# Kernel optimization log

Measured on AMD Instinct MI355X. Metric: run time of the kernel, lower is better.

## Reference

```python
import jax, jax.numpy as jnp
import numpy as np

S, I, CM, C, D, CZ = 128, 512, 256, 32, 32, 128
EPS = 1e-5


def setup_inputs() -> dict:
    key = jax.random.key(0)
    ks = jax.random.split(key, 7)
    x = jax.random.normal(ks[0], (1, S, I, CM), dtype=jnp.float32)
    norm_w = 1.0 + 0.1 * jax.random.normal(ks[1], (CM,), dtype=jnp.float32)
    norm_b = 0.1 * jax.random.normal(ks[2], (CM,), dtype=jnp.float32)
    Wa = jax.random.normal(ks[3], (C, CM), dtype=jnp.float32) / np.sqrt(CM)
    Wb = jax.random.normal(ks[4], (D, CM), dtype=jnp.float32) / np.sqrt(CM)
    Wo = jax.random.normal(ks[5], (CZ, C * D), dtype=jnp.float32) / np.sqrt(C * D)
    bo = 0.1 * jax.random.normal(ks[6], (CZ,), dtype=jnp.float32)
    return {"x": x, "norm_w": norm_w, "norm_b": norm_b, "Wa": Wa, "Wb": Wb, "Wo": Wo, "bo": bo}


def reference(x, norm_w, norm_b, Wa, Wb, Wo, bo):
    m = x[0]                                   # [S, I, CM] (drop leading batch dim)
    mu = jnp.mean(m, axis=-1, keepdims=True)
    var = jnp.mean((m - mu) ** 2, axis=-1, keepdims=True)
    ln = (m - mu) * jax.lax.rsqrt(var + EPS) * norm_w + norm_b
    a = jnp.einsum('sim,cm->sic', ln, Wa)      # [S, I, C]
    b = jnp.einsum('sjm,dm->sjd', ln, Wb)      # [S, J, D]
    s = a.shape[0]
    # outer product mean over S: [I, J, C, D]; flatten order is (c, d) -> c*D + d,
    # matching the reshape(chunk, C, J, D) -> permute(0,2,1,3) -> flatten in the original.
    o = jnp.einsum('sic,sjd->ijcd', a, b) * (1.0 / s)
    z = o.reshape(o.shape[0], o.shape[1], C * D) @ Wo.T + bo  # [I, J, CZ]
    return z[None]                             # [1, I, J, CZ]
```

## Files before the change

kernel.cpp:

```cpp
#include <hip/hip_runtime.h>

#define EPS 1e-5f

typedef _Float16 half8 __attribute__((ext_vector_type(8)));
typedef _Float16 half4 __attribute__((ext_vector_type(4)));
typedef float f32x4 __attribute__((ext_vector_type(4)));

#define AB_STRIDE 72
#define AB_CHUNK  (16384 * AB_STRIDE)

__device__ __forceinline__ void load16_to_lds(const void* g, void* l) {
    __builtin_amdgcn_global_load_lds((__attribute__((address_space(1))) void*)g,
                                     (__attribute__((address_space(3))) void*)l, 16, 0, 0);
}

__global__ void k_cvt(const float* __restrict__ Wo, const float* __restrict__ Wa,
                      const float* __restrict__ Wb, _Float16* __restrict__ WoH,
                      _Float16* __restrict__ WabH)
{
    int t = blockIdx.x * 256 + threadIdx.x;
    if (t < 32768) {
        int n  = t >> 8;
        int k4 = (t & 255) * 4;
        float4 v = *(const float4*)(Wo + (size_t)n * 1024 + k4);
        int c = k4 >> 5, d0 = k4 & 31;
        _Float16* dst = WoH + (size_t)n * 1024 + c;
        dst[(d0 + 0) * 32] = (_Float16)v.x;
        dst[(d0 + 1) * 32] = (_Float16)v.y;
        dst[(d0 + 2) * 32] = (_Float16)v.z;
        dst[(d0 + 3) * 32] = (_Float16)v.w;
    } else {
        int idx = (t - 32768) * 4;
        const float* src = (idx < 8192) ? (Wa + idx) : (Wb + (idx - 8192));
        float4 v = *(const float4*)src;
        half4 h;
        h[0] = (_Float16)v.x; h[1] = (_Float16)v.y; h[2] = (_Float16)v.z; h[3] = (_Float16)v.w;
        *(half4*)(WabH + idx) = h;
    }
}

__global__ __launch_bounds__(512, 4)
void k1_ln_proj(const float* __restrict__ x, const float* __restrict__ nw,
                const float* __restrict__ nb, const _Float16* __restrict__ WabH,
                _Float16* __restrict__ aT, _Float16* __restrict__ bT)
{
    __shared__ _Float16 xln[64 * 264];
    __shared__ _Float16 oT[256 * 72];

    const int tid  = threadIdx.x;
    const int lane = tid & 63;
    const int w    = tid >> 6;
    const int quad = lane >> 4;
    const int l15  = lane & 15;
    const int i0   = (blockIdx.x >> 1) * 4;
    const int sc   = blockIdx.x & 1;

    const int mt  = w & 3;
    const int ntg = w >> 2;

    for (int sub = 0; sub < 4; ++sub) {
        for (int rr = 0; rr < 8; ++rr) {
            int rl = w * 8 + rr;
            int s_ = sc * 64 + sub * 16 + (rl >> 2);
            int i_ = i0 + (rl & 3);
            const float4* xr = (const float4*)(x + ((size_t)s_ * 512 + i_) * 256);
            float4 v = xr[lane];
            float sum = v.x + v.y + v.z + v.w;
            float ss  = v.x * v.x + v.y * v.y + v.z * v.z + v.w * v.w;
            #pragma unroll
            for (int off = 32; off > 0; off >>= 1) {
                sum += __shfl_xor(sum, off);
                ss  += __shfl_xor(ss, off);
            }
            float mu  = sum * (1.f / 256.f);
            float var = ss * (1.f / 256.f) - mu * mu;
            float rs  = rsqrtf(var + EPS);
            float4 gw = ((const float4*)nw)[lane];
            float4 gb = ((const float4*)nb)[lane];
            half4 o;
            o[0] = (_Float16)((v.x - mu) * rs * gw.x + gb.x);
            o[1] = (_Float16)((v.y - mu) * rs * gw.y + gb.y);
            o[2] = (_Float16)((v.z - mu) * rs * gw.z + gb.z);
            o[3] = (_Float16)((v.w - mu) * rs * gw.w + gb.w);
            *(half4*)(xln + rl * 264 + lane * 4) = o;
        }
        __syncthreads();

        f32x4 acc2[2] = {};
        #pragma unroll
        for (int kk = 0; kk < 8; ++kk) {
            half8 af = *(const half8*)(xln + (mt * 16 + l15) * 264 + kk * 32 + quad * 8);
            #pragma unroll
            for (int t = 0; t < 2; ++t) {
                half8 bf = *(const half8*)(WabH + (ntg * 32 + t * 16 + l15) * 256 + kk * 32 + quad * 8);
                acc2[t] = __builtin_amdgcn_mfma_f32_16x16x32_f16(af, bf, acc2[t], 0, 0, 0);
            }
        }

        #pragma unroll
        for (int t = 0; t < 2; ++t) {
            int c64  = ntg * 32 + t * 16 + l15;
            int base = ((c64 >= 32) ? 128 : 0) + (c64 & 31);
            int s_l  = sub * 16 + mt * 4 + quad;
            #pragma unroll
            for (int r = 0; r < 4; ++r)
                oT[(base + r * 32) * 72 + s_l] = (_Float16)acc2[t][r];
        }
        __syncthreads();
    }

    #pragma unroll
    for (int it2 = 0; it2 < 4; ++it2) {
        int u   = it2 * 512 + tid;
        int row = u >> 3;
        int off = (u & 7) * 8;
        half8 v = *(const half8*)(oT + row * 72 + off);
        _Float16* dst = (row < 128) ? aT : bT;
        int grow = i0 * 32 + (row & 127);
        *(half8*)(dst + (size_t)sc * AB_CHUNK + (size_t)grow * 72 + off) = v;
    }
}

__global__ __launch_bounds__(512, 4)
void k2_main(const _Float16* __restrict__ aT, const _Float16* __restrict__ bT,
             const _Float16* __restrict__ WoH, const float* __restrict__ bo,
             float* __restrict__ out)
{
    __shared__ _Float16 smem[33024];
    _Float16* sA = smem;
    _Float16* sB = smem + 256 * AB_STRIDE;
    _Float16* oL = smem;

    const int tid  = threadIdx.x;
    const int lane = tid & 63;
    const int w    = tid >> 6;
    const int quad = lane >> 4;
    const int l15  = lane & 15;
    const int wy   = w >> 1, wx = w & 1;

    const int jt = blockIdx.x, it = blockIdx.y;
    const char* gA = (const char*)(aT + (size_t)it * 256 * AB_STRIDE);
    const char* gB = (const char*)(bT + (size_t)jt * 128 * AB_STRIDE);

    f32x4 acc[4][4] = {};

    for (int ck = 0; ck < 2; ++ck) {
        const char* cA = gA + (size_t)ck * (AB_CHUNK * 2);
        const char* cB = gB + (size_t)ck * (AB_CHUNK * 2);
        for (int seg = w; seg < 54; seg += 8) {
            if (seg < 36) load16_to_lds(cA + seg * 1024 + lane * 16, (char*)sA + seg * 1024 + lane * 16);
            else          load16_to_lds(cB + (seg - 36) * 1024 + lane * 16, (char*)sB + (seg - 36) * 1024 + lane * 16);
        }
        __syncthreads();

        #pragma unroll
        for (int kloc = 0; kloc < 2; ++kloc) {
            half8 af[4], bf[4];
            #pragma unroll
            for (int mt = 0; mt < 4; ++mt)
                af[mt] = *(const half8*)(sA + (wy * 64 + mt * 16 + l15) * AB_STRIDE + kloc * 32 + quad * 8);
            #pragma unroll
            for (int nt = 0; nt < 4; ++nt)
                bf[nt] = *(const half8*)(sB + (wx * 64 + nt * 16 + l15) * AB_STRIDE + kloc * 32 + quad * 8);
            #pragma unroll
            for (int mt = 0; mt < 4; ++mt)
                #pragma unroll
                for (int nt = 0; nt < 4; ++nt)
                    acc[mt][nt] = __builtin_amdgcn_mfma_f32_16x16x32_f16(af[mt], bf[nt], acc[mt][nt], 0, 0, 0);
        }
        __syncthreads();
    }

    #pragma unroll
    for (int mt = 0; mt < 4; ++mt) {
        int c0     = (mt & 1) * 16 + quad * 4;
        int chunk3 = (c0 >> 3);
        int il     = wy * 2 + (mt >> 1);
        #pragma unroll
        for (int nt = 0; nt < 4; ++nt) {
            int d    = (nt & 1) * 16 + l15;
            int jl   = wx * 2 + (nt >> 1);
            int pair = il * 4 + jl;
            int cS   = (c0 & 7) + ((chunk3 ^ ((d >> 1) & 3)) << 3);
            half4 v;
            v[0] = (_Float16)(acc[mt][nt][0] * (1.f / 128.f));
            v[1] = (_Float16)(acc[mt][nt][1] * (1.f / 128.f));
            v[2] = (_Float16)(acc[mt][nt][2] * (1.f / 128.f));
            v[3] = (_Float16)(acc[mt][nt][3] * (1.f / 128.f));
            *(half4*)(oL + pair * 1032 + d * 32 + cS) = v;
        }
    }
    __syncthreads();

    f32x4 zacc[2] = {};
    const int n0 = w * 16 + l15;
    #pragma unroll 4
    for (int kk = 0; kk < 32; ++kk) {
        int csw = (quad ^ ((kk >> 1) & 3)) * 8;
        half8 oa0 = *(const half8*)(oL + (l15) * 1032 + kk * 32 + csw);
        half8 oa1 = *(const half8*)(oL + (16 + l15) * 1032 + kk * 32 + csw);
        half8 w0  = *(const half8*)(WoH + (size_t)n0 * 1024 + kk * 32 + quad * 8);
        zacc[0] = __builtin_amdgcn_mfma_f32_16x16x32_f16(oa0, w0, zacc[0], 0, 0, 0);
        zacc[1] = __builtin_amdgcn_mfma_f32_16x16x32_f16(oa1, w0, zacc[1], 0, 0, 0);
    }

    float bias = bo[w * 16 + l15];
    #pragma unroll
    for (int mt2 = 0; mt2 < 2; ++mt2) {
        #pragma unroll
        for (int r = 0; r < 4; ++r) {
            int il = mt2 * 4 + quad;
            int jl = r;
            out[(((size_t)(it * 8 + il)) * 512 + jt * 4 + jl) * 128 + w * 16 + l15] = zacc[mt2][r] + bias;
        }
    }
}

extern "C" void kernel_launch(void* const* d_in, const int* in_sizes, int n_in,
                              void* d_out, int out_size, void* d_ws, size_t ws_size,
                              hipStream_t stream)
{
    const float* x      = (const float*)d_in[0];
    const float* norm_w = (const float*)d_in[1];
    const float* norm_b = (const float*)d_in[2];
    const float* Wa     = (const float*)d_in[3];
    const float* Wb     = (const float*)d_in[4];
    const float* Wo     = (const float*)d_in[5];
    const float* bo     = (const float*)d_in[6];
    float* out = (float*)d_out;

    _Float16* aT   = (_Float16*)d_ws;
    _Float16* bT   = aT + 2 * (size_t)AB_CHUNK;
    _Float16* WoH  = bT + 2 * (size_t)AB_CHUNK;
    _Float16* WabH = WoH + 131072;

    k_cvt<<<144, 256, 0, stream>>>(Wo, Wa, Wb, WoH, WabH);
    k1_ln_proj<<<256, 512, 0, stream>>>(x, norm_w, norm_b, WabH, aT, bT);
    k2_main<<<dim3(128, 64), 512, 0, stream>>>(aT, bT, WoH, bo, out);
}
```

Baseline: 485.0 us.

## Split LN-projection over more blocks, swizzle k2 grid, prefetch Wo into registers

The LN+projection kernel now gives each block one 16-row S slice instead of looping over four, which quadruples the block count and shrinks the transpose staging buffer. The main kernel becomes a 1D grid remapped into 16x8 tile patches for better L2 reuse of aT/bT. The Wo operand for the final GEMM is double-buffered in registers and prefetched before the outer-product phase. This raises register pressure in k2, which may reduce occupancy.

Result: slower. 517.1 us (+6.6%).

```diff
diff --git a/kernel.cpp b/kernel.cpp
--- a/kernel.cpp
+++ b/kernel.cpp
@@ -39,85 +39,82 @@
     }
 }
 
-__global__ __launch_bounds__(512, 4)
+__global__ __launch_bounds__(512, 6)
 void k1_ln_proj(const float* __restrict__ x, const float* __restrict__ nw,
                 const float* __restrict__ nb, const _Float16* __restrict__ WabH,
                 _Float16* __restrict__ aT, _Float16* __restrict__ bT)
 {
     __shared__ _Float16 xln[64 * 264];
-    __shared__ _Float16 oT[256 * 72];
+    __shared__ _Float16 oT[256 * 24];
 
     const int tid  = threadIdx.x;
     const int lane = tid & 63;
     const int w    = tid >> 6;
     const int quad = lane >> 4;
     const int l15  = lane & 15;
-    const int i0   = (blockIdx.x >> 1) * 4;
-    const int sc   = blockIdx.x & 1;
-
-    const int mt  = w & 3;
-    const int ntg = w >> 2;
-
-    for (int sub = 0; sub < 4; ++sub) {
-        for (int rr = 0; rr < 8; ++rr) {
-            int rl = w * 8 + rr;
-            int s_ = sc * 64 + sub * 16 + (rl >> 2);
-            int i_ = i0 + (rl & 3);
-            const float4* xr = (const float4*)(x + ((size_t)s_ * 512 + i_) * 256);
-            float4 v = xr[lane];
-            float sum = v.x + v.y + v.z + v.w;
-            float ss  = v.x * v.x + v.y * v.y + v.z * v.z + v.w * v.w;
-            #pragma unroll
-            for (int off = 32; off > 0; off >>= 1) {
-                sum += __shfl_xor(sum, off);
-                ss  += __shfl_xor(ss, off);
-            }
-            float mu  = sum * (1.f / 256.f);
-            float var = ss * (1.f / 256.f) - mu * mu;
-            float rs  = rsqrtf(var + EPS);
-            float4 gw = ((const float4*)nw)[lane];
-            float4 gb = ((const float4*)nb)[lane];
-            half4 o;
-            o[0] = (_Float16)((v.x - mu) * rs * gw.x + gb.x);
-            o[1] = (_Float16)((v.y - mu) * rs * gw.y + gb.y);
-            o[2] = (_Float16)((v.z - mu) * rs * gw.z + gb.z);
-            o[3] = (_Float16)((v.w - mu) * rs * gw.w + gb.w);
-            *(half4*)(xln + rl * 264 + lane * 4) = o;
-        }
-        __syncthreads();
-
-        f32x4 acc2[2] = {};
-        #pragma unroll
-        for (int kk = 0; kk < 8; ++kk) {
-            half8 af = *(const half8*)(xln + (mt * 16 + l15) * 264 + kk * 32 + quad * 8);
-            #pragma unroll
-            for (int t = 0; t < 2; ++t) {
-                half8 bf = *(const half8*)(WabH + (ntg * 32 + t * 16 + l15) * 256 + kk * 32 + quad * 8);
-                acc2[t] = __builtin_amdgcn_mfma_f32_16x16x32_f16(af, bf, acc2[t], 0, 0, 0);
-            }
-        }
-
+
+    const int i0   = (blockIdx.x >> 3) * 4;
+    const int s16  = blockIdx.x & 7;
+    const int ck   = s16 >> 2;
+    const int col0 = (s16 & 3) * 16;
+
+    #pragma unroll
+    for (int rr = 0; rr < 8; ++rr) {
+        int rl = w * 8 + rr;
+        int s_ = s16 * 16 + (rl >> 2);
+        int i_ = i0 + (rl & 3);
+        const float4* xr = (const float4*)(x + ((size_t)s_ * 512 + i_) * 256);
+        float4 v = xr[lane];
+        float sum = v.x + v.y + v.z + v.w;
+        float ss  = v.x * v.x + v.y * v.y + v.z * v.z + v.w * v.w;
+        #pragma unroll
+        for (int off = 32; off > 0; off >>= 1) {
+            sum += __shfl_xor(sum, off);
+            ss  += __shfl_xor(ss, off);
+        }
+        float mu  = sum * (1.f / 256.f);
+        float var = ss * (1.f / 256.f) - mu * mu;
+        float rs  = rsqrtf(var + EPS);
+        float4 gw = ((const float4*)nw)[lane];
+        float4 gb = ((const float4*)nb)[lane];
+        half4 o;
+        o[0] = (_Float16)((v.x - mu) * rs * gw.x + gb.x);
+        o[1] = (_Float16)((v.y - mu) * rs * gw.y + gb.y);
+        o[2] = (_Float16)((v.z - mu) * rs * gw.z + gb.z);
+        o[3] = (_Float16)((v.w - mu) * rs * gw.w + gb.w);
+        *(half4*)(xln + rl * 264 + lane * 4) = o;
+    }
+    __syncthreads();
+
+    const int mt = w & 3, ntg = w >> 2;
+    f32x4 acc2[2] = {};
+    #pragma unroll
+    for (int kk = 0; kk < 8; ++kk) {
+        half8 af = *(const half8*)(xln + (mt * 16 + l15) * 264 + kk * 32 + quad * 8);
         #pragma unroll
         for (int t = 0; t < 2; ++t) {
-            int c64  = ntg * 32 + t * 16 + l15;
-            int base = ((c64 >= 32) ? 128 : 0) + (c64 & 31);
-            int s_l  = sub * 16 + mt * 4 + quad;
-            #pragma unroll
-            for (int r = 0; r < 4; ++r)
-                oT[(base + r * 32) * 72 + s_l] = (_Float16)acc2[t][r];
-        }
-        __syncthreads();
-    }
-
-    #pragma unroll
-    for (int it2 = 0; it2 < 4; ++it2) {
-        int u   = it2 * 512 + tid;
-        int row = u >> 3;
-        int off = (u & 7) * 8;
-        half8 v = *(const half8*)(oT + row * 72 + off);
+            half8 bf = *(const half8*)(WabH + (ntg * 32 + t * 16 + l15) * 256 + kk * 32 + quad * 8);
+            acc2[t] = __builtin_amdgcn_mfma_f32_16x16x32_f16(af, bf, acc2[t], 0, 0, 0);
+        }
+    }
+
+    #pragma unroll
+    for (int t = 0; t < 2; ++t) {
+        int c64  = ntg * 32 + t * 16 + l15;
+        int base = ((c64 >= 32) ? 128 : 0) + (c64 & 31);
+        int s_l  = mt * 4 + quad;
+        #pragma unroll
+        for (int r = 0; r < 4; ++r)
+            oT[(base + r * 32) * 24 + s_l] = (_Float16)acc2[t][r];
+    }
+    __syncthreads();
+
+    {
+        int row = tid >> 1, h = tid & 1;
+        half8 v = *(const half8*)(oT + row * 24 + h * 8);
         _Float16* dst = (row < 128) ? aT : bT;
         int grow = i0 * 32 + (row & 127);
-        *(half8*)(dst + (size_t)sc * AB_CHUNK + (size_t)grow * 72 + off) = v;
+        *(half8*)(dst + (size_t)ck * AB_CHUNK + (size_t)grow * 72 + col0 + h * 8) = v;
     }
 }
 
@@ -138,7 +135,18 @@
     const int l15  = lane & 15;
     const int wy   = w >> 1, wx = w & 1;
 
-    const int jt = blockIdx.x, it = blockIdx.y;
+    const int bid    = blockIdx.x;
+    const int patch  = bid >> 7, within = bid & 127;
+    const int jt = ((patch & 7) << 4) | (within & 15);
+    const int it = ((patch >> 3) << 3) | (within >> 4);
+
+    const int n0 = w * 16 + l15;
+    const _Float16* wp = WoH + (size_t)n0 * 1024 + quad * 8;
+    half8 wreg[2][4];
+    #pragma unroll
+    for (int u = 0; u < 4; ++u) wreg[0][u] = *(const half8*)(wp + u * 32);
+    const float bias = bo[n0];
+
     const char* gA = (const char*)(aT + (size_t)it * 256 * AB_STRIDE);
     const char* gB = (const char*)(bT + (size_t)jt * 128 * AB_STRIDE);
 
@@ -193,25 +201,32 @@
     __syncthreads();
 
     f32x4 zacc[2] = {};
-    const int n0 = w * 16 + l15;
-    #pragma unroll 4
-    for (int kk = 0; kk < 32; ++kk) {
-        int csw = (quad ^ ((kk >> 1) & 3)) * 8;
-        half8 oa0 = *(const half8*)(oL + (l15) * 1032 + kk * 32 + csw);
-        half8 oa1 = *(const half8*)(oL + (16 + l15) * 1032 + kk * 32 + csw);
-        half8 w0  = *(const half8*)(WoH + (size_t)n0 * 1024 + kk * 32 + quad * 8);
-        zacc[0] = __builtin_amdgcn_mfma_f32_16x16x32_f16(oa0, w0, zacc[0], 0, 0, 0);
-        zacc[1] = __builtin_amdgcn_mfma_f32_16x16x32_f16(oa1, w0, zacc[1], 0, 0, 0);
-    }
-
-    float bias = bo[w * 16 + l15];
+    #pragma unroll
+    for (int g = 0; g < 8; ++g) {
+        int cur = g & 1;
+        if (g < 7) {
+            #pragma unroll
+            for (int u = 0; u < 4; ++u)
+                wreg[cur ^ 1][u] = *(const half8*)(wp + (g + 1) * 128 + u * 32);
+        }
+        #pragma unroll
+        for (int u = 0; u < 4; ++u) {
+            int kk  = g * 4 + u;
+            int csw = (quad ^ ((kk >> 1) & 3)) * 8;
+            half8 oa0 = *(const half8*)(oL + l15 * 1032 + kk * 32 + csw);
+            half8 oa1 = *(const half8*)(oL + (16 + l15) * 1032 + kk * 32 + csw);
+            zacc[0] = __builtin_amdgcn_mfma_f32_16x16x32_f16(oa0, wreg[cur][u], zacc[0], 0, 0, 0);
+            zacc[1] = __builtin_amdgcn_mfma_f32_16x16x32_f16(oa1, wreg[cur][u], zacc[1], 0, 0, 0);
+        }
+    }
+
     #pragma unroll
     for (int mt2 = 0; mt2 < 2; ++mt2) {
         #pragma unroll
         for (int r = 0; r < 4; ++r) {
             int il = mt2 * 4 + quad;
             int jl = r;
-            out[(((size_t)(it * 8 + il)) * 512 + jt * 4 + jl) * 128 + w * 16 + l15] = zacc[mt2][r] + bias;
+            out[(((size_t)(it * 8 + il)) * 512 + jt * 4 + jl) * 128 + n0 - l15 + l15] = zacc[mt2][r] + bias;
         }
     }
 }
@@ -235,6 +250,6 @@
     _Float16* WabH = WoH + 131072;
 
     k_cvt<<<144, 256, 0, stream>>>(Wo, Wa, Wb, WoH, WabH);
-    k1_ln_proj<<<256, 512, 0, stream>>>(x, norm_w, norm_b, WabH, aT, bT);
-    k2_main<<<dim3(128, 64), 512, 0, stream>>>(aT, bT, WoH, bo, out);
-}
+    k1_ln_proj<<<1024, 512, 0, stream>>>(x, norm_w, norm_b, WabH, aT, bT);
+    k2_main<<<8192, 512, 0, stream>>>(aT, bT, WoH, bo, out);
+}
```
